# Kernel tuning notes

Measured on AMD Instinct MI355X. Metric: run time of the kernel, lower is better.

The kernel has to match this reference:

```python
import jax, jax.numpy as jnp
import numpy as np

B, T, DIM = 2, 2048, 1024
H, HD = 16, 64          # num_heads, head_dim (DIM = H*HD)
SCALE = 0.12            # fixed attn_scale in the module
ROPE_BASE = 1024.0
EPS = 1e-6


def _rope_tables(seq_len, head_dim):
    half = head_dim // 2
    keep = head_dim // 4
    active = (1.0 / ROPE_BASE) ** jnp.linspace(0.0, 1.0, keep, dtype=jnp.float32)
    inv_freq = jnp.concatenate([active, jnp.zeros(half - keep, dtype=jnp.float32)])
    theta = jnp.arange(seq_len, dtype=jnp.float32)[:, None] * inv_freq[None, :]  # [T, half]
    return jnp.cos(theta), jnp.sin(theta)


def _rms_norm(x):
    # F.rms_norm without learned scale
    return x * jax.lax.rsqrt(jnp.mean(x * x, axis=-1, keepdims=True) + EPS)


def _apply_rope(x_bthd, cos, sin):
    # x_bthd: [B,T,H,HD]; cos/sin: [T, HD/2]
    xf = x_bthd.astype(jnp.float32)
    x1, x2 = jnp.split(xf, 2, axis=-1)
    c = cos[None, :, None, :]
    s = sin[None, :, None, :]
    y = jnp.concatenate([x1 * c + x2 * s, -x1 * s + x2 * c], axis=-1)
    return y.astype(x_bthd.dtype)


def setup_inputs() -> dict:
    key = jax.random.key(0)
    k1, k2, k3, k4 = jax.random.split(key, 4)
    x = jax.random.normal(k1, (B, T, DIM), dtype=jnp.float32)
    ve = jax.random.normal(k2, (B, T, DIM), dtype=jnp.float32)
    sa_lambdas = jax.random.uniform(k3, (2,), dtype=jnp.float32)
    # additive causal mask, as SDPA receives a float mask cast to q dtype
    causal = jnp.tril(jnp.ones((T, T), dtype=bool))
    attn_mask = jnp.where(causal, 0.0, -1e9).astype(jnp.float32)[None, None]
    # qkvo weights; scaled like a typical linear init (original zero-inits W_o,
    # here kept random so the output is non-trivial for kernel testing)
    qkvo_w = jax.random.normal(k4, (4, DIM, DIM), dtype=jnp.float32) * (DIM ** -0.5)
    return {"x": x, "ve": ve, "sa_lambdas": sa_lambdas, "attn_mask": attn_mask, "qkvo_w": qkvo_w}


def reference(x, ve, sa_lambdas, attn_mask, qkvo_w):
    b, t, _ = x.shape
    # fused QKV projection: qkvo_w[:3] is [3, DIM, DIM], F.linear -> x @ W.T
    qkv = jnp.einsum('btd,ked->btke', x, qkvo_w[:3])          # [B,T,3,DIM]
    q = _rms_norm(qkv[:, :, 0].reshape(b, t, H, HD))
    k = _rms_norm(qkv[:, :, 1].reshape(b, t, H, HD))
    v = _rms_norm(qkv[:, :, 2].reshape(b, t, H, HD))
    cos, sin = _rope_tables(t, HD)
    q = _apply_rope(q, cos, sin)
    k = _apply_rope(k, cos, sin)
    # value-embedding blend
    v = sa_lambdas[0] * v + sa_lambdas[1] * ve.reshape(b, t, H, HD)
    # attention with fixed scale and additive mask
    scores = jnp.einsum('bthd,bshd->bhts', q, k) * SCALE + attn_mask
    att = jax.nn.softmax(scores, axis=-1)
    y = jnp.einsum('bhts,bshd->bthd', att, v).reshape(b, t, DIM)
    return y @ qkvo_w[3].T
```

## Files before the change

### kernel.cpp

```cpp
#include <hip/hip_runtime.h>
#include <hip/hip_bf16.h>
#include <stdint.h>

#define T_SEQ 2048
#define DIMSZ 1024
#define NH    16
#define HDIM  64
#define NBATCH 2
#define KVB   64
#define ATT_SCALE 0.12f
#define QSCALE (0.12f * 1.4426950408889634f)

typedef __attribute__((ext_vector_type(8))) __bf16 bf16x8;
typedef __attribute__((ext_vector_type(8))) ushort u16x8;
typedef __attribute__((ext_vector_type(4))) float f32x4;

#define GLOAD_LDS16(gp, lp)                                                            \
  __builtin_amdgcn_global_load_lds((const __attribute__((address_space(1))) void*)(gp),\
                                   (__attribute__((address_space(3))) void*)(lp),      \
                                   16, 0, 0)

__device__ __forceinline__ ushort f2bf(float f) {
  union { float f; uint32_t u; } v; v.f = f;
  uint32_t u = v.u;
  uint32_t r = (u + 0x7FFFu + ((u >> 16) & 1u)) >> 16;
  return (ushort)r;
}

__device__ __forceinline__ float bf2f(ushort h) {
  union { float f; uint32_t u; } v;
  v.u = ((uint32_t)h) << 16;
  return v.f;
}

__device__ __forceinline__ uint32_t pk2(float a, float b) {
  union { __hip_bfloat162 h; uint32_t u; } cv;
  cv.h = __hip_bfloat162(__float2bfloat16(a), __float2bfloat16(b));
  return cv.u;
}

__global__ __launch_bounds__(256) void conv_bf16_k(const float* __restrict__ in,
                                                   ushort* __restrict__ out, int n) {
  int i = (blockIdx.x * 256 + threadIdx.x) * 4;
  if (i >= n) return;
  float4 v = *(const float4*)(in + i);
  ushort4 o;
  o.x = f2bf(v.x); o.y = f2bf(v.y); o.z = f2bf(v.z); o.w = f2bf(v.w);
  *(ushort4*)(out + i) = o;
}

__global__ __launch_bounds__(256) void rope_tab_k(float* __restrict__ ctab,
                                                  float* __restrict__ stab) {
  int idx = blockIdx.x * 256 + threadIdx.x;
  if (idx >= T_SEQ * 32) return;
  int j = idx & 31, t = idx >> 5;
  float c = 1.f, s = 0.f;
  if (j < 16) {
    float inv = powf(1024.0f, -(float)j / 15.0f);
    float th = (float)t * inv;
    c = cosf(th);
    s = sinf(th);
  }
  ctab[idx] = c;
  stab[idx] = s;
}

#define BM 128
#define BN 128
#define BKS 64

__global__ __launch_bounds__(256) void gemm_out_k(const ushort* __restrict__ A,
                                                  const ushort* __restrict__ Bt,
                                                  float* __restrict__ C) {
  const int K = DIMSZ, N = DIMSZ;
  __shared__ __align__(16) ushort As[64 * BKS];
  __shared__ __align__(16) ushort Bs[128 * BKS];
  int tid = threadIdx.x;
  int wave = tid >> 6, lane = tid & 63;
  int lr = lane & 15, lg = lane >> 4;
  int m0 = blockIdx.x * 64, n0 = blockIdx.y * 128;
  int wm = (wave >> 1) * 32, wn = (wave & 1) * 64;

  int srow = tid >> 3;
  int sel = (((tid & 7) ^ (srow & 7)) << 3);

  f32x4 acc[2][4];
#pragma unroll
  for (int m = 0; m < 2; ++m)
#pragma unroll
    for (int n = 0; n < 4; ++n)
      acc[m][n] = (f32x4){0.f, 0.f, 0.f, 0.f};

  for (int k0 = 0; k0 < K; k0 += BKS) {
#pragma unroll
    for (int it = 0; it < 2; ++it)
      GLOAD_LDS16(A + (size_t)(m0 + it * 32 + srow) * K + k0 + sel, &As[(it * 256 + tid) * 8]);
#pragma unroll
    for (int it = 0; it < 4; ++it)
      GLOAD_LDS16(Bt + (size_t)(n0 + it * 32 + srow) * K + k0 + sel, &Bs[(it * 256 + tid) * 8]);
    __syncthreads();
#pragma unroll
    for (int kk = 0; kk < 2; ++kk) {
      int cA = (((kk * 4 + lg) ^ (lr & 7)) << 3);
      bf16x8 af[2], bf[4];
#pragma unroll
      for (int m = 0; m < 2; ++m)
        af[m] = *(const bf16x8*)&As[(wm + m * 16 + lr) * BKS + cA];
#pragma unroll
      for (int n = 0; n < 4; ++n)
        bf[n] = *(const bf16x8*)&Bs[(wn + n * 16 + lr) * BKS + cA];
#pragma unroll
      for (int m = 0; m < 2; ++m)
#pragma unroll
        for (int n = 0; n < 4; ++n)
          acc[m][n] = __builtin_amdgcn_mfma_f32_16x16x32_bf16(af[m], bf[n], acc[m][n], 0, 0, 0);
    }
    __syncthreads();
  }
#pragma unroll
  for (int m = 0; m < 2; ++m)
#pragma unroll
    for (int n = 0; n < 4; ++n)
#pragma unroll
      for (int r = 0; r < 4; ++r) {
        int row = m0 + wm + m * 16 + lg * 4 + r;
        int col = n0 + wn + n * 16 + lr;
        C[(size_t)row * N + col] = acc[m][n][r];
      }
}

__global__ __launch_bounds__(256) void gemm_qkv_k(const ushort* __restrict__ A,
                                                  const ushort* __restrict__ Bt,
                                                  const float* __restrict__ ve,
                                                  const float* __restrict__ lam,
                                                  const float* __restrict__ ctab,
                                                  const float* __restrict__ stab,
                                                  ushort* __restrict__ Qb,
                                                  ushort* __restrict__ Kb,
                                                  ushort* __restrict__ Vt) {
  const int K = DIMSZ;
  __shared__ __align__(16) ushort As[BM * BKS];
  __shared__ __align__(16) ushort Bs[BN * BKS];
  int tid = threadIdx.x;
  int wave = tid >> 6, lane = tid & 63;
  int lr = lane & 15, lg = lane >> 4;
  int m0 = blockIdx.x * BM, n0 = blockIdx.y * BN;
  int wm = (wave >> 1) * 64, wn = (wave & 1) * 64;

  int srow = tid >> 3;
  int sel = (((tid & 7) ^ (srow & 7)) << 3);

  f32x4 acc[4][4];
  for (int m = 0; m < 4; ++m)
    for (int n = 0; n < 4; ++n)
      acc[m][n] = (f32x4){0.f, 0.f, 0.f, 0.f};

  for (int k0 = 0; k0 < K; k0 += BKS) {
#pragma unroll
    for (int it = 0; it < 4; ++it) {
      GLOAD_LDS16(A + (size_t)(m0 + it * 32 + srow) * K + k0 + sel, &As[(it * 256 + tid) * 8]);
      GLOAD_LDS16(Bt + (size_t)(n0 + it * 32 + srow) * K + k0 + sel, &Bs[(it * 256 + tid) * 8]);
    }
    __syncthreads();
#pragma unroll
    for (int kk = 0; kk < 2; ++kk) {
      int cA = (((kk * 4 + lg) ^ (lr & 7)) << 3);
      bf16x8 af[4], bf[4];
#pragma unroll
      for (int m = 0; m < 4; ++m)
        af[m] = *(const bf16x8*)&As[(wm + m * 16 + lr) * BKS + cA];
#pragma unroll
      for (int n = 0; n < 4; ++n)
        bf[n] = *(const bf16x8*)&Bs[(wn + n * 16 + lr) * BKS + cA];
#pragma unroll
      for (int m = 0; m < 4; ++m)
#pragma unroll
        for (int n = 0; n < 4; ++n)
          acc[m][n] = __builtin_amdgcn_mfma_f32_16x16x32_bf16(af[m], bf[n], acc[m][n], 0, 0, 0);
    }
    __syncthreads();
  }

  int sec = n0 >> 10;
  int h = ((n0 & 1023) + wn) >> 6;
  ushort* Tl = (wave < 2 ? As : Bs) + (wave & 1) * 4096;

#pragma unroll
  for (int m = 0; m < 4; ++m)
#pragma unroll
    for (int n = 0; n < 4; ++n)
#pragma unroll
      for (int r = 0; r < 4; ++r) {
        int tl = m * 16 + lg * 4 + r;
        int d = n * 16 + lr;
        Tl[tl * 64 + ((((d >> 3) ^ (tl & 7)) << 3) | (d & 7))] = f2bf(acc[m][n][r]);
      }

  int tl = lane;
  float xv[64];
#pragma unroll
  for (int j = 0; j < 8; ++j) {
    u16x8 rw = *(const u16x8*)&Tl[tl * 64 + ((j ^ (tl & 7)) << 3)];
#pragma unroll
    for (int e = 0; e < 8; ++e) xv[j * 8 + e] = bf2f((ushort)rw[e]);
  }

  float ss = 0.f;
#pragma unroll
  for (int i = 0; i < 64; ++i) ss += xv[i] * xv[i];
  float rinv = rsqrtf(ss * (1.0f / 64.0f) + 1e-6f);
#pragma unroll
  for (int i = 0; i < 64; ++i) xv[i] *= rinv;

  int row = m0 + wm + tl;
  int t = row & (T_SEQ - 1);
  int bb = row >> 11;
  int bh = bb * NH + h;

  if (sec < 2) {
    float cs[16], sn[16];
    const float4* cp = (const float4*)(ctab + t * 32);
    const float4* sp = (const float4*)(stab + t * 32);
#pragma unroll
    for (int j = 0; j < 4; ++j) {
      float4 c4 = cp[j], s4 = sp[j];
      cs[j * 4 + 0] = c4.x; cs[j * 4 + 1] = c4.y; cs[j * 4 + 2] = c4.z; cs[j * 4 + 3] = c4.w;
      sn[j * 4 + 0] = s4.x; sn[j * 4 + 1] = s4.y; sn[j * 4 + 2] = s4.z; sn[j * 4 + 3] = s4.w;
    }
#pragma unroll
    for (int j = 0; j < 16; ++j) {
      float a = xv[j], bv = xv[j + 32];
      xv[j] = a * cs[j] + bv * sn[j];
      xv[j + 32] = bv * cs[j] - a * sn[j];
    }
    float sc = (sec == 0) ? QSCALE : 1.0f;
    ushort* dst = (sec == 0 ? Qb : Kb) + ((size_t)bh * T_SEQ + t) * HDIM;
#pragma unroll
    for (int p = 0; p < 8; ++p) {
      uint4 wq = make_uint4(pk2(xv[8 * p] * sc, xv[8 * p + 1] * sc),
                            pk2(xv[8 * p + 2] * sc, xv[8 * p + 3] * sc),
                            pk2(xv[8 * p + 4] * sc, xv[8 * p + 5] * sc),
                            pk2(xv[8 * p + 6] * sc, xv[8 * p + 7] * sc));
      *((uint4*)dst + p) = wq;
    }
  } else {
    float l0 = lam[0], l1 = lam[1];
    const float4* vp = (const float4*)(ve + ((size_t)(bb * T_SEQ + t)) * DIMSZ + h * HDIM);
#pragma unroll
    for (int j = 0; j < 16; ++j) {
      float4 vv4 = vp[j];
      xv[j * 4 + 0] = l0 * xv[j * 4 + 0] + l1 * vv4.x;
      xv[j * 4 + 1] = l0 * xv[j * 4 + 1] + l1 * vv4.y;
      xv[j * 4 + 2] = l0 * xv[j * 4 + 2] + l1 * vv4.z;
      xv[j * 4 + 3] = l0 * xv[j * 4 + 3] + l1 * vv4.w;
    }
    ushort* dst = Vt + (size_t)bh * HDIM * T_SEQ + t;
#pragma unroll
    for (int i = 0; i < 64; ++i)
      dst[(size_t)i * T_SEQ] = f2bf(xv[i]);
  }
}

__global__ __launch_bounds__(256, 3) void attn_k(const ushort* __restrict__ Q,
                                                 const ushort* __restrict__ K,
                                                 const ushort* __restrict__ Vt,
                                                 ushort* __restrict__ Y) {
  int bh = blockIdx.x;
  int qb = 31 - blockIdx.y;
  int tid = threadIdx.x;
  int wid = tid >> 6, lane = tid & 63;
  int lr = lane & 15, lg = lane >> 4;
  int b = bh >> 4, h = bh & 15;

  int r0 = qb * 64 + wid * 16;
  int nkv = qb + 1;

  __shared__ __align__(16) ushort Kl[2][KVB * HDIM];
  __shared__ __align__(16) ushort Vl[2][KVB * HDIM];
  __shared__ __align__(16) ushort Plds[4][16][72];

  const ushort* Kbh = K + (size_t)bh * T_SEQ * HDIM;
  const ushort* Vbh = Vt + (size_t)bh * HDIM * T_SEQ;

  int sr = tid >> 3;
  int sel = (((tid & 7) ^ (sr & 7)) << 3);
  const ushort* ksrc0 = Kbh + (size_t)sr * HDIM + sel;
  const ushort* ksrc1 = Kbh + (size_t)(sr + 32) * HDIM + sel;
  const ushort* vsrc0 = Vbh + (size_t)sr * T_SEQ + sel;
  const ushort* vsrc1 = Vbh + (size_t)(sr + 32) * T_SEQ + sel;
  int ld0 = tid * 8, ld1 = tid * 8 + 2048;

  const ushort* Qbase = Q + ((size_t)bh * T_SEQ + r0) * HDIM;
  bf16x8 aq[2];
#pragma unroll
  for (int kk = 0; kk < 2; ++kk)
    aq[kk] = *(const bf16x8*)(Qbase + (size_t)lr * HDIM + kk * 32 + lg * 8);

  int fcol[2];
  fcol[0] = ((0 + lg) ^ (lr & 7)) << 3;
  fcol[1] = ((4 + lg) ^ (lr & 7)) << 3;

  f32x4 o[4];
#pragma unroll
  for (int n = 0; n < 4; ++n) o[n] = (f32x4){0.f, 0.f, 0.f, 0.f};
  float lrow = 0.f;

  GLOAD_LDS16(ksrc0, &Kl[0][ld0]);
  GLOAD_LDS16(ksrc1, &Kl[0][ld1]);
  GLOAD_LDS16(vsrc0, &Vl[0][ld0]);
  GLOAD_LDS16(vsrc1, &Vl[0][ld1]);
  __syncthreads();

  for (int kb = 0; kb < nkv; ++kb) {
    int cur = kb & 1;
    if (kb + 1 < nkv) {
      size_t ko = (size_t)(kb + 1) * KVB * HDIM;
      int vo = (kb + 1) * KVB;
      GLOAD_LDS16(ksrc0 + ko, &Kl[cur ^ 1][ld0]);
      GLOAD_LDS16(ksrc1 + ko, &Kl[cur ^ 1][ld1]);
      GLOAD_LDS16(vsrc0 + vo, &Vl[cur ^ 1][ld0]);
      GLOAD_LDS16(vsrc1 + vo, &Vl[cur ^ 1][ld1]);
    }
    const ushort* Kc = &Kl[cur][0];
    const ushort* Vc = &Vl[cur][0];
    f32x4 s[4];
#pragma unroll
    for (int n = 0; n < 4; ++n) {
      f32x4 a = (f32x4){0.f, 0.f, 0.f, 0.f};
      bf16x8 kf0 = *(const bf16x8*)&Kc[(n * 16 + lr) * HDIM + fcol[0]];
      a = __builtin_amdgcn_mfma_f32_16x16x32_bf16(kf0, aq[0], a, 0, 0, 0);
      bf16x8 kf1 = *(const bf16x8*)&Kc[(n * 16 + lr) * HDIM + fcol[1]];
      a = __builtin_amdgcn_mfma_f32_16x16x32_bf16(kf1, aq[1], a, 0, 0, 0);
      s[n] = a;
    }
    if (kb == nkv - 1) {
      int qrow = r0 + lr;
      int kb0 = kb * KVB + lg * 4;
#pragma unroll
      for (int n = 0; n < 4; ++n)
#pragma unroll
        for (int r = 0; r < 4; ++r)
          if (kb0 + n * 16 + r > qrow) s[n][r] = -1e30f;
    }
    float psum = 0.f;
#pragma unroll
    for (int n = 0; n < 4; ++n) {
      float p0 = exp2f(s[n][0]), p1 = exp2f(s[n][1]);
      float p2 = exp2f(s[n][2]), p3 = exp2f(s[n][3]);
      psum += (p0 + p1) + (p2 + p3);
      uint2 w;
      w.x = pk2(p0, p1);
      w.y = pk2(p2, p3);
      *(uint2*)&Plds[wid][lr][n * 16 + lg * 4] = w;
    }
    lrow += psum;
#pragma unroll
    for (int kk = 0; kk < 2; ++kk) {
      bf16x8 ap = *(const bf16x8*)&Plds[wid][lr][kk * 32 + lg * 8];
#pragma unroll
      for (int n = 0; n < 4; ++n) {
        bf16x8 vf = *(const bf16x8*)&Vc[(n * 16 + lr) * HDIM + fcol[kk]];
        o[n] = __builtin_amdgcn_mfma_f32_16x16x32_bf16(vf, ap, o[n], 0, 0, 0);
      }
    }
    __syncthreads();
  }
  lrow += __shfl_xor(lrow, 16);
  lrow += __shfl_xor(lrow, 32);
  float inv = 1.0f / lrow;
  int row = r0 + lr;
#pragma unroll
  for (int n = 0; n < 4; ++n) {
    uint2 w;
    w.x = pk2(o[n][0] * inv, o[n][1] * inv);
    w.y = pk2(o[n][2] * inv, o[n][3] * inv);
    *(uint2*)&Y[((size_t)b * T_SEQ + row) * DIMSZ + h * HDIM + n * 16 + lg * 4] = w;
  }
}

extern "C" void kernel_launch(void* const* d_in, const int* in_sizes, int n_in,
                              void* d_out, int out_size, void* d_ws, size_t ws_size,
                              hipStream_t stream) {
  const float* x   = (const float*)d_in[0];
  const float* ve  = (const float*)d_in[1];
  const float* lam = (const float*)d_in[2];
  const float* w   = (const float*)d_in[4];
  float* out = (float*)d_out;

  char* ws = (char*)d_ws;
  const size_t NTOK = (size_t)NBATCH * T_SEQ;
  const size_t nX = NTOK * DIMSZ;
  const size_t nW = 4ull * DIMSZ * DIMSZ;

  ushort* Xb   = (ushort*)(ws);
  ushort* Wb   = (ushort*)(ws + 8388608);
  ushort* Qb   = (ushort*)(ws + 16777216);
  ushort* Kb   = (ushort*)(ws + 25165824);
  ushort* Vt   = (ushort*)(ws + 33554432);
  ushort* Yb   = (ushort*)(ws + 41943040);
  float*  ctab = (float*)(ws + 50331648);
  float*  stab = (float*)(ws + 50593792);

  conv_bf16_k<<<(int)(nX / 4 / 256), 256, 0, stream>>>(x, Xb, (int)nX);
  conv_bf16_k<<<(int)(nW / 4 / 256), 256, 0, stream>>>(w, Wb, (int)nW);
  rope_tab_k<<<(T_SEQ * 32) / 256, 256, 0, stream>>>(ctab, stab);

  gemm_qkv_k<<<dim3(4096 / BM, 3072 / BN), 256, 0, stream>>>(Xb, Wb, ve, lam, ctab, stab,
                                                             Qb, Kb, Vt);

  attn_k<<<dim3(NBATCH * NH, 32), 256, 0, stream>>>(Qb, Kb, Vt, Yb);

  gemm_out_k<<<dim3(4096 / 64, 1024 / 128), 256, 0, stream>>>(Yb, Wb + 3ull * DIMSZ * DIMSZ, out);
}
```

Baseline: 120.9 us.

## Split QKV epilogue into separate post-kernel and merge prep kernels

Merges the three preparation kernels (x and weight bf16 conversion, RoPE tables) into one launch. The QKV GEMM epilogue, which did RMSNorm, RoPE, value blending and a transposed V store, is moved out into a separate per-head wave kernel that reads a bf16 QKV buffer from global memory. This is meant to lighten the GEMM epilogue and its register use, and to remove the strided per-thread V transpose writes. In exchange it adds a full round trip of the QKV intermediate through global memory and one extra launch.

```diff
diff --git a/kernel.cpp b/kernel.cpp
--- a/kernel.cpp
+++ b/kernel.cpp
@@ -39,35 +39,149 @@
   return cv.u;
 }
 
-__global__ __launch_bounds__(256) void conv_bf16_k(const float* __restrict__ in,
-                                                   ushort* __restrict__ out, int n) {
-  int i = (blockIdx.x * 256 + threadIdx.x) * 4;
-  if (i >= n) return;
-  float4 v = *(const float4*)(in + i);
-  ushort4 o;
-  o.x = f2bf(v.x); o.y = f2bf(v.y); o.z = f2bf(v.z); o.w = f2bf(v.w);
-  *(ushort4*)(out + i) = o;
-}
-
-__global__ __launch_bounds__(256) void rope_tab_k(float* __restrict__ ctab,
-                                                  float* __restrict__ stab) {
-  int idx = blockIdx.x * 256 + threadIdx.x;
-  if (idx >= T_SEQ * 32) return;
-  int j = idx & 31, t = idx >> 5;
-  float c = 1.f, s = 0.f;
-  if (j < 16) {
-    float inv = powf(1024.0f, -(float)j / 15.0f);
-    float th = (float)t * inv;
-    c = cosf(th);
-    s = sinf(th);
-  }
-  ctab[idx] = c;
-  stab[idx] = s;
+__global__ __launch_bounds__(256) void prep_k(const float* __restrict__ x,
+                                              const float* __restrict__ w,
+                                              ushort* __restrict__ Xb,
+                                              ushort* __restrict__ Wb,
+                                              float* __restrict__ ctab,
+                                              float* __restrict__ stab) {
+  int bid = blockIdx.x;
+  int tid = threadIdx.x;
+  if (bid < 4096) {
+    int i = (bid * 256 + tid) * 4;
+    float4 v = *(const float4*)(x + i);
+    ushort4 o;
+    o.x = f2bf(v.x); o.y = f2bf(v.y); o.z = f2bf(v.z); o.w = f2bf(v.w);
+    *(ushort4*)(Xb + i) = o;
+  } else if (bid < 8192) {
+    int i = ((bid - 4096) * 256 + tid) * 4;
+    float4 v = *(const float4*)(w + i);
+    ushort4 o;
+    o.x = f2bf(v.x); o.y = f2bf(v.y); o.z = f2bf(v.z); o.w = f2bf(v.w);
+    *(ushort4*)(Wb + i) = o;
+  } else {
+    int idx = (bid - 8192) * 256 + tid;
+    int j = idx & 31, t = idx >> 5;
+    float c = 1.f, s = 0.f;
+    if (j < 16) {
+      float inv = powf(1024.0f, -(float)j / 15.0f);
+      float th = (float)t * inv;
+      c = cosf(th);
+      s = sinf(th);
+    }
+    ctab[idx] = c;
+    stab[idx] = s;
+  }
 }
 
 #define BM 128
 #define BN 128
 #define BKS 64
+
+__global__ __launch_bounds__(256) void gemm_qkvc_k(const ushort* __restrict__ A,
+                                                   const ushort* __restrict__ Bt,
+                                                   ushort* __restrict__ C) {
+  const int K = DIMSZ, N = 3 * DIMSZ;
+  __shared__ __align__(16) ushort As[BM * BKS];
+  __shared__ __align__(16) ushort Bs[BN * BKS];
+  int tid = threadIdx.x;
+  int wave = tid >> 6, lane = tid & 63;
+  int lr = lane & 15, lg = lane >> 4;
+  int m0 = blockIdx.x * BM, n0 = blockIdx.y * BN;
+  int wm = (wave >> 1) * 64, wn = (wave & 1) * 64;
+
+  int srow = tid >> 3;
+  int sel = (((tid & 7) ^ (srow & 7)) << 3);
+
+  f32x4 acc[4][4];
+  for (int m = 0; m < 4; ++m)
+    for (int n = 0; n < 4; ++n)
+      acc[m][n] = (f32x4){0.f, 0.f, 0.f, 0.f};
+
+  for (int k0 = 0; k0 < K; k0 += BKS) {
+#pragma unroll
+    for (int it = 0; it < 4; ++it) {
+      GLOAD_LDS16(A + (size_t)(m0 + it * 32 + srow) * K + k0 + sel, &As[(it * 256 + tid) * 8]);
+      GLOAD_LDS16(Bt + (size_t)(n0 + it * 32 + srow) * K + k0 + sel, &Bs[(it * 256 + tid) * 8]);
+    }
+    __syncthreads();
+#pragma unroll
+    for (int kk = 0; kk < 2; ++kk) {
+      int cA = (((kk * 4 + lg) ^ (lr & 7)) << 3);
+      bf16x8 af[4], bf[4];
+#pragma unroll
+      for (int m = 0; m < 4; ++m)
+        af[m] = *(const bf16x8*)&As[(wm + m * 16 + lr) * BKS + cA];
+#pragma unroll
+      for (int n = 0; n < 4; ++n)
+        bf[n] = *(const bf16x8*)&Bs[(wn + n * 16 + lr) * BKS + cA];
+#pragma unroll
+      for (int m = 0; m < 4; ++m)
+#pragma unroll
+        for (int n = 0; n < 4; ++n)
+          acc[m][n] = __builtin_amdgcn_mfma_f32_16x16x32_bf16(af[m], bf[n], acc[m][n], 0, 0, 0);
+    }
+    __syncthreads();
+  }
+#pragma unroll
+  for (int m = 0; m < 4; ++m)
+#pragma unroll
+    for (int n = 0; n < 4; ++n)
+#pragma unroll
+      for (int r = 0; r < 4; ++r) {
+        int row = m0 + wm + m * 16 + lg * 4 + r;
+        int col = n0 + wn + n * 16 + lr;
+        C[(size_t)row * N + col] = f2bf(acc[m][n][r]);
+      }
+}
+
+__global__ __launch_bounds__(256) void qkv_post_k(const ushort* __restrict__ QKVb,
+                                                  const float* __restrict__ ve,
+                                                  const float* __restrict__ lam,
+                                                  const float* __restrict__ ctab,
+                                                  const float* __restrict__ stab,
+                                                  ushort* __restrict__ Qb,
+                                                  ushort* __restrict__ Kb,
+                                                  ushort* __restrict__ Vt) {
+  int idx = blockIdx.x * 4 + (threadIdx.x >> 6);
+  int lane = threadIdx.x & 63;
+  int h = idx & (NH - 1);
+  int bt = idx >> 4;
+  int t = bt & (T_SEQ - 1);
+  int b = bt >> 11;
+
+  const ushort* base = QKVb + (size_t)bt * 3072 + h * HDIM + lane;
+  float qv = bf2f(base[0]);
+  float kv = bf2f(base[1024]);
+  float vv = bf2f(base[2048]);
+
+  float sq = qv * qv, sk = kv * kv, sv = vv * vv;
+#pragma unroll
+  for (int off = 1; off < 64; off <<= 1) {
+    sq += __shfl_xor(sq, off);
+    sk += __shfl_xor(sk, off);
+    sv += __shfl_xor(sv, off);
+  }
+  qv *= rsqrtf(sq * (1.0f / 64.0f) + 1e-6f);
+  kv *= rsqrtf(sk * (1.0f / 64.0f) + 1e-6f);
+  vv *= rsqrtf(sv * (1.0f / 64.0f) + 1e-6f);
+
+  int j = lane & 31;
+  float c = ctab[t * 32 + j];
+  float s = stab[t * 32 + j];
+  float qo = __shfl_xor(qv, 32);
+  float ko = __shfl_xor(kv, 32);
+  float q2 = (lane < 32) ? (qv * c + qo * s) : (qv * c - qo * s);
+  float k2 = (lane < 32) ? (kv * c + ko * s) : (kv * c - ko * s);
+  float v2 = lam[0] * vv + lam[1] * ve[(size_t)bt * DIMSZ + h * HDIM + lane];
+
+  q2 *= QSCALE;
+
+  int bh = b * NH + h;
+  Qb[((size_t)bh * T_SEQ + t) * HDIM + lane] = f2bf(q2);
+  Kb[((size_t)bh * T_SEQ + t) * HDIM + lane] = f2bf(k2);
+  Vt[((size_t)bh * HDIM + lane) * T_SEQ + t] = f2bf(v2);
+}
 
 __global__ __launch_bounds__(256) void gemm_out_k(const ushort* __restrict__ A,
                                                   const ushort* __restrict__ Bt,
@@ -129,138 +243,6 @@
       }
 }
 
-__global__ __launch_bounds__(256) void gemm_qkv_k(const ushort* __restrict__ A,
-                                                  const ushort* __restrict__ Bt,
-                                                  const float* __restrict__ ve,
-                                                  const float* __restrict__ lam,
-                                                  const float* __restrict__ ctab,
-                                                  const float* __restrict__ stab,
-                                                  ushort* __restrict__ Qb,
-                                                  ushort* __restrict__ Kb,
-                                                  ushort* __restrict__ Vt) {
-  const int K = DIMSZ;
-  __shared__ __align__(16) ushort As[BM * BKS];
-  __shared__ __align__(16) ushort Bs[BN * BKS];
-  int tid = threadIdx.x;
-  int wave = tid >> 6, lane = tid & 63;
-  int lr = lane & 15, lg = lane >> 4;
-  int m0 = blockIdx.x * BM, n0 = blockIdx.y * BN;
-  int wm = (wave >> 1) * 64, wn = (wave & 1) * 64;
-
-  int srow = tid >> 3;
-  int sel = (((tid & 7) ^ (srow & 7)) << 3);
-
-  f32x4 acc[4][4];
-  for (int m = 0; m < 4; ++m)
-    for (int n = 0; n < 4; ++n)
-      acc[m][n] = (f32x4){0.f, 0.f, 0.f, 0.f};
-
-  for (int k0 = 0; k0 < K; k0 += BKS) {
-#pragma unroll
-    for (int it = 0; it < 4; ++it) {
-      GLOAD_LDS16(A + (size_t)(m0 + it * 32 + srow) * K + k0 + sel, &As[(it * 256 + tid) * 8]);
-      GLOAD_LDS16(Bt + (size_t)(n0 + it * 32 + srow) * K + k0 + sel, &Bs[(it * 256 + tid) * 8]);
-    }
-    __syncthreads();
-#pragma unroll
-    for (int kk = 0; kk < 2; ++kk) {
-      int cA = (((kk * 4 + lg) ^ (lr & 7)) << 3);
-      bf16x8 af[4], bf[4];
-#pragma unroll
-      for (int m = 0; m < 4; ++m)
-        af[m] = *(const bf16x8*)&As[(wm + m * 16 + lr) * BKS + cA];
-#pragma unroll
-      for (int n = 0; n < 4; ++n)
-        bf[n] = *(const bf16x8*)&Bs[(wn + n * 16 + lr) * BKS + cA];
-#pragma unroll
-      for (int m = 0; m < 4; ++m)
-#pragma unroll
-        for (int n = 0; n < 4; ++n)
-          acc[m][n] = __builtin_amdgcn_mfma_f32_16x16x32_bf16(af[m], bf[n], acc[m][n], 0, 0, 0);
-    }
-    __syncthreads();
-  }
-
-  int sec = n0 >> 10;
-  int h = ((n0 & 1023) + wn) >> 6;
-  ushort* Tl = (wave < 2 ? As : Bs) + (wave & 1) * 4096;
-
-#pragma unroll
-  for (int m = 0; m < 4; ++m)
-#pragma unroll
-    for (int n = 0; n < 4; ++n)
-#pragma unroll
-      for (int r = 0; r < 4; ++r) {
-        int tl = m * 16 + lg * 4 + r;
-        int d = n * 16 + lr;
-        Tl[tl * 64 + ((((d >> 3) ^ (tl & 7)) << 3) | (d & 7))] = f2bf(acc[m][n][r]);
-      }
-
-  int tl = lane;
-  float xv[64];
-#pragma unroll
-  for (int j = 0; j < 8; ++j) {
-    u16x8 rw = *(const u16x8*)&Tl[tl * 64 + ((j ^ (tl & 7)) << 3)];
-#pragma unroll
-    for (int e = 0; e < 8; ++e) xv[j * 8 + e] = bf2f((ushort)rw[e]);
-  }
-
-  float ss = 0.f;
-#pragma unroll
-  for (int i = 0; i < 64; ++i) ss += xv[i] * xv[i];
-  float rinv = rsqrtf(ss * (1.0f / 64.0f) + 1e-6f);
-#pragma unroll
-  for (int i = 0; i < 64; ++i) xv[i] *= rinv;
-
-  int row = m0 + wm + tl;
-  int t = row & (T_SEQ - 1);
-  int bb = row >> 11;
-  int bh = bb * NH + h;
-
-  if (sec < 2) {
-    float cs[16], sn[16];
-    const float4* cp = (const float4*)(ctab + t * 32);
-    const float4* sp = (const float4*)(stab + t * 32);
-#pragma unroll
-    for (int j = 0; j < 4; ++j) {
-      float4 c4 = cp[j], s4 = sp[j];
-      cs[j * 4 + 0] = c4.x; cs[j * 4 + 1] = c4.y; cs[j * 4 + 2] = c4.z; cs[j * 4 + 3] = c4.w;
-      sn[j * 4 + 0] = s4.x; sn[j * 4 + 1] = s4.y; sn[j * 4 + 2] = s4.z; sn[j * 4 + 3] = s4.w;
-    }
-#pragma unroll
-    for (int j = 0; j < 16; ++j) {
-      float a = xv[j], bv = xv[j + 32];
-      xv[j] = a * cs[j] + bv * sn[j];
-      xv[j + 32] = bv * cs[j] - a * sn[j];
-    }
-    float sc = (sec == 0) ? QSCALE : 1.0f;
-    ushort* dst = (sec == 0 ? Qb : Kb) + ((size_t)bh * T_SEQ + t) * HDIM;
-#pragma unroll
-    for (int p = 0; p < 8; ++p) {
-      uint4 wq = make_uint4(pk2(xv[8 * p] * sc, xv[8 * p + 1] * sc),
-                            pk2(xv[8 * p + 2] * sc, xv[8 * p + 3] * sc),
-                            pk2(xv[8 * p + 4] * sc, xv[8 * p + 5] * sc),
-                            pk2(xv[8 * p + 6] * sc, xv[8 * p + 7] * sc));
-      *((uint4*)dst + p) = wq;
-    }
-  } else {
-    float l0 = lam[0], l1 = lam[1];
-    const float4* vp = (const float4*)(ve + ((size_t)(bb * T_SEQ + t)) * DIMSZ + h * HDIM);
-#pragma unroll
-    for (int j = 0; j < 16; ++j) {
-      float4 vv4 = vp[j];
-      xv[j * 4 + 0] = l0 * xv[j * 4 + 0] + l1 * vv4.x;
-      xv[j * 4 + 1] = l0 * xv[j * 4 + 1] + l1 * vv4.y;
-      xv[j * 4 + 2] = l0 * xv[j * 4 + 2] + l1 * vv4.z;
-      xv[j * 4 + 3] = l0 * xv[j * 4 + 3] + l1 * vv4.w;
-    }
-    ushort* dst = Vt + (size_t)bh * HDIM * T_SEQ + t;
-#pragma unroll
-    for (int i = 0; i < 64; ++i)
-      dst[(size_t)i * T_SEQ] = f2bf(xv[i]);
-  }
-}
-
 __global__ __launch_bounds__(256, 3) void attn_k(const ushort* __restrict__ Q,
                                                  const ushort* __restrict__ K,
                                                  const ushort* __restrict__ Vt,
@@ -389,24 +371,22 @@
 
   char* ws = (char*)d_ws;
   const size_t NTOK = (size_t)NBATCH * T_SEQ;
-  const size_t nX = NTOK * DIMSZ;
-  const size_t nW = 4ull * DIMSZ * DIMSZ;
 
   ushort* Xb   = (ushort*)(ws);
   ushort* Wb   = (ushort*)(ws + 8388608);
-  ushort* Qb   = (ushort*)(ws + 16777216);
-  ushort* Kb   = (ushort*)(ws + 25165824);
-  ushort* Vt   = (ushort*)(ws + 33554432);
-  ushort* Yb   = (ushort*)(ws + 41943040);
-  float*  ctab = (float*)(ws + 50331648);
-  float*  stab = (float*)(ws + 50593792);
-
-  conv_bf16_k<<<(int)(nX / 4 / 256), 256, 0, stream>>>(x, Xb, (int)nX);
-  conv_bf16_k<<<(int)(nW / 4 / 256), 256, 0, stream>>>(w, Wb, (int)nW);
-  rope_tab_k<<<(T_SEQ * 32) / 256, 256, 0, stream>>>(ctab, stab);
-
-  gemm_qkv_k<<<dim3(4096 / BM, 3072 / BN), 256, 0, stream>>>(Xb, Wb, ve, lam, ctab, stab,
-                                                             Qb, Kb, Vt);
+  ushort* QKVb = (ushort*)(ws + 16777216);
+  ushort* Qb   = (ushort*)(ws + 41943040);
+  ushort* Kb   = (ushort*)(ws + 50331648);
+  ushort* Vt   = (ushort*)(ws + 58720256);
+  ushort* Yb   = (ushort*)(ws + 67108864);
+  float*  ctab = (float*)(ws + 75497472);
+  float*  stab = (float*)(ws + 75759616);
+
+  prep_k<<<8448, 256, 0, stream>>>(x, w, Xb, Wb, ctab, stab);
+
+  gemm_qkvc_k<<<dim3(4096 / BM, 3072 / BN), 256, 0, stream>>>(Xb, Wb, QKVb);
+
+  qkv_post_k<<<(int)(NTOK * NH / 4), 256, 0, stream>>>(QKVb, ve, lam, ctab, stab, Qb, Kb, Vt);
 
   attn_k<<<dim3(NBATCH * NH, 32), 256, 0, stream>>>(Qb, Kb, Vt, Yb);
 
```

Measured after the change: 126.9 us. 5.0% more time.
